# Kernel optimization log

Measured on AMD Instinct MI355X. Metric: run time of the kernel, lower is better.

Reference implementation:

```python
import jax, jax.numpy as jnp
import numpy as np


def setup_inputs() -> dict:
    key = jax.random.key(0)
    k1, k2, k3 = jax.random.split(key, 3)
    B, I, O = 2048, 256, 512
    x = jax.random.normal(k1, (B, I), dtype=jnp.float32)
    weight = jax.random.normal(k2, (O, I, 2), dtype=jnp.float32) * 0.1
    bias = jax.random.normal(k3, (O, I + 1), dtype=jnp.float32) * 0.1
    return {"x": x, "weight": weight, "bias": bias}


def reference(x, weight, bias):
    # out[b, o] = sum_i weight[o, i, 0] * sin(weight[o, i, 1] * x[b, i] + bias[o, i]) + bias[o, -1]
    w_out = weight[:, :, 0]          # [O, I]
    w_sin = weight[:, :, 1]          # [O, I]
    b_sin = bias[:, :-1]             # [O, I]
    b_out = bias[:, -1]              # [O]
    # [B, O, I] intermediate: sin applied before the reduction over in_features
    trig = jnp.sin(x[:, None, :] * w_sin[None, :, :] + b_sin[None, :, :])
    out = jnp.einsum('oi,boi->bo', w_out, trig) + b_out[None, :]
    return out
```

## Files before the change

### kernel.cpp

```cpp
#include <hip/hip_runtime.h>


#define B_SZ 2048
#define I_SZ 256
#define O_SZ 512
#define BTILE 64
#define ITILE 128
#define OBLOCK 16
#define NOO 4

static constexpr float kInv2Pi = 0.15915494309189535f;

__global__ __launch_bounds__(256, 4) void TrigoLinear_kernel(
    const float* __restrict__ x, const float* __restrict__ w,
    const float* __restrict__ bias, float* __restrict__ out) {
  __shared__ float xT[ITILE][BTILE + 1];

  const int tid = threadIdx.x;
  const int lane = tid & 63;
  const int wave = __builtin_amdgcn_readfirstlane(tid >> 6);

  const int btile = blockIdx.x & 31;
  const int oblock = blockIdx.x >> 5;
  const int b0 = btile * BTILE;
  const int o_base = oblock * OBLOCK + wave * NOO;

  float acc[NOO] = {0.f, 0.f, 0.f, 0.f};

  for (int it = 0; it < I_SZ / ITILE; ++it) {
    __syncthreads();
#pragma unroll
    for (int k = 0; k < 32; ++k) {
      int e = tid + k * 256;
      int row = e >> 7;
      int col = e & 127;
      xT[col][row] = x[(b0 + row) * I_SZ + it * ITILE + col] * kInv2Pi;
    }
    __syncthreads();

#pragma unroll 4
    for (int i = 0; i < ITILE; ++i) {
      const float xs = xT[i][lane];
      const int ig = it * ITILE + i;
#pragma unroll
      for (int oo = 0; oo < NOO; ++oo) {
        const int o = o_base + oo;
        const float wov = w[o * (2 * I_SZ) + 2 * ig];
        const float wsv = w[o * (2 * I_SZ) + 2 * ig + 1];
        const float bsv = bias[o * (I_SZ + 1) + ig];
        float t = xs * wsv;
        float rev = __builtin_fmaf(bsv, kInv2Pi, t);
        float r = __builtin_amdgcn_fractf(rev);
        float sv = __builtin_amdgcn_sinf(r);
        acc[oo] = __builtin_fmaf(sv, wov, acc[oo]);
      }
    }
  }

  const int b = b0 + lane;
#pragma unroll
  for (int oo = 0; oo < NOO; ++oo) {
    const int o = o_base + oo;
    const float bout = bias[o * (I_SZ + 1) + I_SZ];
    out[b * O_SZ + o] = acc[oo] + bout;
  }
}

extern "C" void kernel_launch(void* const* d_in, const int* in_sizes, int n_in,
                              void* d_out, int out_size, void* d_ws, size_t ws_size,
                              hipStream_t stream) {
  const float* x = (const float*)d_in[0];
  const float* w = (const float*)d_in[1];
  const float* bias = (const float*)d_in[2];
  float* out = (float*)d_out;

  const int grid = (B_SZ / BTILE) * (O_SZ / OBLOCK);
  TrigoLinear_kernel<<<dim3(grid), dim3(256), 0, stream>>>(x, w, bias, out);
}
```

Before: 53.08 us.

## Pre-scale weights in a prep kernel, drop fract, and shrink tiles

Adds a prep kernel that splits the interleaved weights into planar arrays. The sin-frequency and phase arrays are pre-multiplied by 1/(2π), so the inner loop becomes a single fma feeding the hardware sin, and the explicit fract range reduction is removed. The main kernel also moves to smaller I/O tiles (ITILE 64, 2 outputs per wave), a higher launch-bounds occupancy hint, and float4 loads when staging x. This trades an extra kernel launch and a workspace round-trip for fewer VALU ops per element. Dropping fract relies on the hardware sin tolerating unreduced arguments.

```diff
diff --git a/kernel.cpp b/kernel.cpp
--- a/kernel.cpp
+++ b/kernel.cpp
@@ -5,15 +5,29 @@
 #define I_SZ 256
 #define O_SZ 512
 #define BTILE 64
-#define ITILE 128
-#define OBLOCK 16
-#define NOO 4
+#define ITILE 64
+#define OBLOCK 8
+#define NOO 2
 
 static constexpr float kInv2Pi = 0.15915494309189535f;
 
-__global__ __launch_bounds__(256, 4) void TrigoLinear_kernel(
-    const float* __restrict__ x, const float* __restrict__ w,
-    const float* __restrict__ bias, float* __restrict__ out) {
+__global__ __launch_bounds__(256) void prep_kernel(
+    const float* __restrict__ w, const float* __restrict__ bias,
+    float* __restrict__ A, float* __restrict__ Bm, float* __restrict__ C) {
+  const int o = blockIdx.x;
+  const int i = threadIdx.x;
+  const float2 wp = *reinterpret_cast<const float2*>(&w[o * (2 * I_SZ) + 2 * i]);
+  A[o * I_SZ + i] = wp.y * kInv2Pi;
+  Bm[o * I_SZ + i] = wp.x;
+  C[o * I_SZ + i] = bias[o * (I_SZ + 1) + i] * kInv2Pi;
+}
+
+template <bool PREPPED>
+__global__ __launch_bounds__(256, 8) void TrigoLinear_kernel(
+    const float* __restrict__ x, const float* __restrict__ A,
+    const float* __restrict__ Bm, const float* __restrict__ C,
+    const float* __restrict__ w, const float* __restrict__ bias,
+    float* __restrict__ out) {
   __shared__ float xT[ITILE][BTILE + 1];
 
   const int tid = threadIdx.x;
@@ -25,34 +39,50 @@
   const int b0 = btile * BTILE;
   const int o_base = oblock * OBLOCK + wave * NOO;
 
-  float acc[NOO] = {0.f, 0.f, 0.f, 0.f};
+  float acc[NOO] = {0.f, 0.f};
 
   for (int it = 0; it < I_SZ / ITILE; ++it) {
     __syncthreads();
 #pragma unroll
-    for (int k = 0; k < 32; ++k) {
-      int e = tid + k * 256;
-      int row = e >> 7;
-      int col = e & 127;
-      xT[col][row] = x[(b0 + row) * I_SZ + it * ITILE + col] * kInv2Pi;
+    for (int c = 0; c < 4; ++c) {
+      const int idx = tid + c * 256;
+      const int row = idx >> 4;
+      const int col = (idx & 15) * 4;
+      float4 v = *reinterpret_cast<const float4*>(
+          &x[(b0 + row) * I_SZ + it * ITILE + col]);
+      if (!PREPPED) {
+        v.x *= kInv2Pi; v.y *= kInv2Pi; v.z *= kInv2Pi; v.w *= kInv2Pi;
+      }
+      xT[col + 0][row] = v.x;
+      xT[col + 1][row] = v.y;
+      xT[col + 2][row] = v.z;
+      xT[col + 3][row] = v.w;
     }
     __syncthreads();
 
-#pragma unroll 4
+#pragma unroll 8
     for (int i = 0; i < ITILE; ++i) {
       const float xs = xT[i][lane];
       const int ig = it * ITILE + i;
 #pragma unroll
       for (int oo = 0; oo < NOO; ++oo) {
         const int o = o_base + oo;
-        const float wov = w[o * (2 * I_SZ) + 2 * ig];
-        const float wsv = w[o * (2 * I_SZ) + 2 * ig + 1];
-        const float bsv = bias[o * (I_SZ + 1) + ig];
-        float t = xs * wsv;
-        float rev = __builtin_fmaf(bsv, kInv2Pi, t);
-        float r = __builtin_amdgcn_fractf(rev);
-        float sv = __builtin_amdgcn_sinf(r);
-        acc[oo] = __builtin_fmaf(sv, wov, acc[oo]);
+        if (PREPPED) {
+          const float a = A[o * I_SZ + ig];
+          const float bo = Bm[o * I_SZ + ig];
+          const float c = C[o * I_SZ + ig];
+          const float rev = __builtin_fmaf(xs, a, c);
+          const float sv = __builtin_amdgcn_sinf(rev);
+          acc[oo] = __builtin_fmaf(sv, bo, acc[oo]);
+        } else {
+          const float wov = w[o * (2 * I_SZ) + 2 * ig];
+          const float wsv = w[o * (2 * I_SZ) + 2 * ig + 1];
+          const float bsv = bias[o * (I_SZ + 1) + ig];
+          const float t = xs * wsv;
+          const float rev = __builtin_fmaf(bsv, kInv2Pi, t);
+          const float sv = __builtin_amdgcn_sinf(rev);
+          acc[oo] = __builtin_fmaf(sv, wov, acc[oo]);
+        }
       }
     }
   }
@@ -61,8 +91,7 @@
 #pragma unroll
   for (int oo = 0; oo < NOO; ++oo) {
     const int o = o_base + oo;
-    const float bout = bias[o * (I_SZ + 1) + I_SZ];
-    out[b * O_SZ + o] = acc[oo] + bout;
+    out[b * O_SZ + o] = acc[oo] + bias[o * (I_SZ + 1) + I_SZ];
   }
 }
 
@@ -75,5 +104,17 @@
   float* out = (float*)d_out;
 
   const int grid = (B_SZ / BTILE) * (O_SZ / OBLOCK);
-  TrigoLinear_kernel<<<dim3(grid), dim3(256), 0, stream>>>(x, w, bias, out);
+  const size_t need = (size_t)3 * O_SZ * I_SZ * sizeof(float);
+
+  if (ws_size >= need) {
+    float* A = (float*)d_ws;
+    float* Bm = A + O_SZ * I_SZ;
+    float* C = Bm + O_SZ * I_SZ;
+    prep_kernel<<<dim3(O_SZ), dim3(I_SZ), 0, stream>>>(w, bias, A, Bm, C);
+    TrigoLinear_kernel<true><<<dim3(grid), dim3(256), 0, stream>>>(
+        x, A, Bm, C, w, bias, out);
+  } else {
+    TrigoLinear_kernel<false><<<dim3(grid), dim3(256), 0, stream>>>(
+        x, nullptr, nullptr, nullptr, w, bias, out);
+  }
 }
```

New measurement: 55.77 us. 1.05x slower.

## Prepack weights into workspace and read x rows directly with register prefetch

Applied to the files above, without the earlier changes.

Adds a prep kernel that repacks the weight and bias into pre-scaled float4/float2 arrays in the workspace, so the main loop does one FMA per sin and drops the fract range reduction. The main kernel no longer stages x through shared memory: each lane reads its own x row as float4 with double-buffered register prefetch. Each wave now computes 2 outputs with 4 accumulators, and occupancy is raised to 6 blocks per CU. Removing fract relies on the hardware sin accepting unreduced arguments. The extra launch and strided per-lane x loads may cost bandwidth in exchange.

```diff
diff --git a/kernel.cpp b/kernel.cpp
--- a/kernel.cpp
+++ b/kernel.cpp
@@ -4,66 +4,108 @@
 #define B_SZ 2048
 #define I_SZ 256
 #define O_SZ 512
-#define BTILE 64
-#define ITILE 128
-#define OBLOCK 16
-#define NOO 4
 
 static constexpr float kInv2Pi = 0.15915494309189535f;
 
-__global__ __launch_bounds__(256, 4) void TrigoLinear_kernel(
-    const float* __restrict__ x, const float* __restrict__ w,
+__global__ __launch_bounds__(128) void prep_kernel(
+    const float* __restrict__ w, const float* __restrict__ bias,
+    float4* __restrict__ AC, float2* __restrict__ W) {
+  const int o = blockIdx.x;
+  const int i2 = threadIdx.x;
+  const float4 wq = *reinterpret_cast<const float4*>(&w[o * 2 * I_SZ + 4 * i2]);
+  const float b0 = bias[o * (I_SZ + 1) + 2 * i2];
+  const float b1 = bias[o * (I_SZ + 1) + 2 * i2 + 1];
+  AC[o * 128 + i2] =
+      make_float4(wq.y * kInv2Pi, wq.w * kInv2Pi, b0 * kInv2Pi, b1 * kInv2Pi);
+  W[o * 128 + i2] = make_float2(wq.x, wq.z);
+}
+
+template <bool PREPPED>
+__global__ __launch_bounds__(256, 6) void TrigoLinear_kernel(
+    const float* __restrict__ x, const float4* __restrict__ AC,
+    const float2* __restrict__ W, const float* __restrict__ w_raw,
     const float* __restrict__ bias, float* __restrict__ out) {
-  __shared__ float xT[ITILE][BTILE + 1];
-
   const int tid = threadIdx.x;
   const int lane = tid & 63;
   const int wave = __builtin_amdgcn_readfirstlane(tid >> 6);
 
   const int btile = blockIdx.x & 31;
-  const int oblock = blockIdx.x >> 5;
-  const int b0 = btile * BTILE;
-  const int o_base = oblock * OBLOCK + wave * NOO;
+  const int ogrp = blockIdx.x >> 5;
+  const int o0 = __builtin_amdgcn_readfirstlane(ogrp * 8 + wave * 2);
+  const int o1 = o0 + 1;
+  const int b = btile * 64 + lane;
 
-  float acc[NOO] = {0.f, 0.f, 0.f, 0.f};
+  const float4* __restrict__ xrow =
+      reinterpret_cast<const float4*>(x + (size_t)b * I_SZ);
 
-  for (int it = 0; it < I_SZ / ITILE; ++it) {
-    __syncthreads();
+  const float4* __restrict__ AC0 = AC + (size_t)o0 * 128;
+  const float4* __restrict__ AC1 = AC + (size_t)o1 * 128;
+  const float2* __restrict__ W0 = W + (size_t)o0 * 128;
+  const float2* __restrict__ W1 = W + (size_t)o1 * 128;
+  const float4* __restrict__ WR0 =
+      reinterpret_cast<const float4*>(w_raw + (size_t)o0 * 2 * I_SZ);
+  const float4* __restrict__ WR1 =
+      reinterpret_cast<const float4*>(w_raw + (size_t)o1 * 2 * I_SZ);
+  const float* __restrict__ BR0 = bias + (size_t)o0 * (I_SZ + 1);
+  const float* __restrict__ BR1 = bias + (size_t)o1 * (I_SZ + 1);
+
+  float acc00 = 0.f, acc01 = 0.f;
+  float acc10 = 0.f, acc11 = 0.f;
+
+  auto process = [&](int c, const float4* xq) {
 #pragma unroll
-    for (int k = 0; k < 32; ++k) {
-      int e = tid + k * 256;
-      int row = e >> 7;
-      int col = e & 127;
-      xT[col][row] = x[(b0 + row) * I_SZ + it * ITILE + col] * kInv2Pi;
-    }
-    __syncthreads();
-
-#pragma unroll 4
-    for (int i = 0; i < ITILE; ++i) {
-      const float xs = xT[i][lane];
-      const int ig = it * ITILE + i;
-#pragma unroll
-      for (int oo = 0; oo < NOO; ++oo) {
-        const int o = o_base + oo;
-        const float wov = w[o * (2 * I_SZ) + 2 * ig];
-        const float wsv = w[o * (2 * I_SZ) + 2 * ig + 1];
-        const float bsv = bias[o * (I_SZ + 1) + ig];
-        float t = xs * wsv;
-        float rev = __builtin_fmaf(bsv, kInv2Pi, t);
-        float r = __builtin_amdgcn_fractf(rev);
-        float sv = __builtin_amdgcn_sinf(r);
-        acc[oo] = __builtin_fmaf(sv, wov, acc[oo]);
+    for (int q = 0; q < 8; ++q) {
+      const float4 xv = xq[q >> 1];
+      const float xe = (q & 1) ? xv.z : xv.x;
+      const float xo = (q & 1) ? xv.w : xv.y;
+      const int i2 = c * 8 + q;
+      if (PREPPED) {
+        const float4 ac0 = AC0[i2];
+        const float4 ac1 = AC1[i2];
+        const float2 wv0 = W0[i2];
+        const float2 wv1 = W1[i2];
+        acc00 = __builtin_fmaf(
+            __builtin_amdgcn_sinf(__builtin_fmaf(xe, ac0.x, ac0.z)), wv0.x, acc00);
+        acc01 = __builtin_fmaf(
+            __builtin_amdgcn_sinf(__builtin_fmaf(xo, ac0.y, ac0.w)), wv0.y, acc01);
+        acc10 = __builtin_fmaf(
+            __builtin_amdgcn_sinf(__builtin_fmaf(xe, ac1.x, ac1.z)), wv1.x, acc10);
+        acc11 = __builtin_fmaf(
+            __builtin_amdgcn_sinf(__builtin_fmaf(xo, ac1.y, ac1.w)), wv1.y, acc11);
+      } else {
+        const float4 wq0 = WR0[i2];
+        const float4 wq1 = WR1[i2];
+        const float be0 = BR0[2 * i2], bo0 = BR0[2 * i2 + 1];
+        const float be1 = BR1[2 * i2], bo1 = BR1[2 * i2 + 1];
+        float t;
+        t = __builtin_fmaf(xe, wq0.y, be0) * kInv2Pi;
+        acc00 = __builtin_fmaf(__builtin_amdgcn_sinf(t), wq0.x, acc00);
+        t = __builtin_fmaf(xo, wq0.w, bo0) * kInv2Pi;
+        acc01 = __builtin_fmaf(__builtin_amdgcn_sinf(t), wq0.z, acc01);
+        t = __builtin_fmaf(xe, wq1.y, be1) * kInv2Pi;
+        acc10 = __builtin_fmaf(__builtin_amdgcn_sinf(t), wq1.x, acc10);
+        t = __builtin_fmaf(xo, wq1.w, bo1) * kInv2Pi;
+        acc11 = __builtin_fmaf(__builtin_amdgcn_sinf(t), wq1.z, acc11);
       }
     }
+  };
+
+  float4 xq[4], xn[4];
+#pragma unroll
+  for (int k = 0; k < 4; ++k) xq[k] = xrow[k];
+
+#pragma unroll 1
+  for (int c = 0; c < 15; ++c) {
+#pragma unroll
+    for (int k = 0; k < 4; ++k) xn[k] = xrow[(c + 1) * 4 + k];
+    process(c, xq);
+#pragma unroll
+    for (int k = 0; k < 4; ++k) xq[k] = xn[k];
   }
+  process(15, xq);
 
-  const int b = b0 + lane;
-#pragma unroll
-  for (int oo = 0; oo < NOO; ++oo) {
-    const int o = o_base + oo;
-    const float bout = bias[o * (I_SZ + 1) + I_SZ];
-    out[b * O_SZ + o] = acc[oo] + bout;
-  }
+  out[(size_t)b * O_SZ + o0] = acc00 + acc01 + bias[(size_t)o0 * (I_SZ + 1) + I_SZ];
+  out[(size_t)b * O_SZ + o1] = acc10 + acc11 + bias[(size_t)o1 * (I_SZ + 1) + I_SZ];
 }
 
 extern "C" void kernel_launch(void* const* d_in, const int* in_sizes, int n_in,
@@ -74,6 +116,18 @@
   const float* bias = (const float*)d_in[2];
   float* out = (float*)d_out;
 
-  const int grid = (B_SZ / BTILE) * (O_SZ / OBLOCK);
-  TrigoLinear_kernel<<<dim3(grid), dim3(256), 0, stream>>>(x, w, bias, out);
+  const int grid = (B_SZ / 64) * (O_SZ / 8);
+  const size_t needAC = (size_t)O_SZ * 128 * sizeof(float4);
+  const size_t needW = (size_t)O_SZ * 128 * sizeof(float2);
+
+  if (ws_size >= needAC + needW) {
+    float4* AC = (float4*)d_ws;
+    float2* W = (float2*)((char*)d_ws + needAC);
+    prep_kernel<<<dim3(O_SZ), dim3(128), 0, stream>>>(w, bias, AC, W);
+    TrigoLinear_kernel<true><<<dim3(grid), dim3(256), 0, stream>>>(
+        x, AC, W, w, bias, out);
+  } else {
+    TrigoLinear_kernel<false><<<dim3(grid), dim3(256), 0, stream>>>(
+        x, nullptr, nullptr, w, bias, out);
+  }
 }
```

Result: slower. 78.29 us (+47.5%).

## Prepack weights into planar arrays and use register-pipelined vector loads with packed FMA

Applied to the files above, without the earlier changes.

A prep kernel splits the interleaved weight and bias into three contiguous planes (sin scale, phase and output weight), with the 1/2π factor folded in. This lets the main kernel use float4 loads. The main kernel drops LDS staging of x. Each lane instead reads its own x row with float4 loads, double-buffered in registers, and computes two outputs per wave using packed 2-wide FMAs. The fract range reduction is removed, which relies on the hardware sin handling the small arguments directly. In exchange it adds an extra kernel launch and workspace traffic, and x reuse now depends on the cache rather than shared memory.

```diff
diff --git a/kernel.cpp b/kernel.cpp
--- a/kernel.cpp
+++ b/kernel.cpp
@@ -4,66 +4,122 @@
 #define B_SZ 2048
 #define I_SZ 256
 #define O_SZ 512
-#define BTILE 64
-#define ITILE 128
-#define OBLOCK 16
-#define NOO 4
 
+typedef float f32x2 __attribute__((ext_vector_type(2)));
 static constexpr float kInv2Pi = 0.15915494309189535f;
 
-__global__ __launch_bounds__(256, 4) void TrigoLinear_kernel(
+static __device__ __forceinline__ f32x2 mk2(float a, float b) {
+  f32x2 r; r.x = a; r.y = b; return r;
+}
+#if __has_builtin(__builtin_elementwise_fma)
+static __device__ __forceinline__ f32x2 fma2(f32x2 a, f32x2 b, f32x2 c) {
+  return __builtin_elementwise_fma(a, b, c);
+}
+#else
+static __device__ __forceinline__ f32x2 fma2(f32x2 a, f32x2 b, f32x2 c) {
+  return mk2(__builtin_fmaf(a.x, b.x, c.x), __builtin_fmaf(a.y, b.y, c.y));
+}
+#endif
+static __device__ __forceinline__ f32x2 sin2(f32x2 v) {
+  return mk2(__builtin_amdgcn_sinf(v.x), __builtin_amdgcn_sinf(v.y));
+}
+
+__global__ __launch_bounds__(256) void prep_kernel(
+    const float* __restrict__ w, const float* __restrict__ bias,
+    float* __restrict__ A, float* __restrict__ C, float* __restrict__ W) {
+  const int o = blockIdx.x;
+  const int i = threadIdx.x;
+  const float2 wp = *reinterpret_cast<const float2*>(&w[(size_t)o * 2 * I_SZ + 2 * i]);
+  A[o * I_SZ + i] = wp.y * kInv2Pi;
+  C[o * I_SZ + i] = bias[o * (I_SZ + 1) + i] * kInv2Pi;
+  W[o * I_SZ + i] = wp.x;
+}
+
+__global__ __launch_bounds__(256, 6) void TrigoLinear_kernel(
+    const float* __restrict__ x, const float* __restrict__ A,
+    const float* __restrict__ C, const float* __restrict__ W,
+    const float* __restrict__ bias, float* __restrict__ out) {
+  const int tid = threadIdx.x;
+  const int lane = tid & 63;
+  const int wave = tid >> 6;
+  const int btile = blockIdx.x & 31;
+  const int og = blockIdx.x >> 5;
+  const int o0 = og * 8 + wave * 2;
+  const int b = btile * 64 + lane;
+
+  int opq0;
+  asm("v_mov_b32 %0, 0" : "=v"(opq0));
+  const int wi = o0 * I_SZ + opq0;
+  const int xi = b * I_SZ;
+
+  f32x2 acc0a = mk2(0.f, 0.f), acc0b = mk2(0.f, 0.f);
+  f32x2 acc1a = mk2(0.f, 0.f), acc1b = mk2(0.f, 0.f);
+
+  float4 Px, Pa0, Pc0, Pw0, Pa1, Pc1, Pw1;
+  float4 Qx, Qa0, Qc0, Qw0, Qa1, Qc1, Qw1;
+
+#define LD4(base, off) (*reinterpret_cast<const float4*>((base) + (off)))
+#define STAGE(S, cc)                                            \
+  do {                                                          \
+    const int _o = (cc) << 2;                                   \
+    S##x  = LD4(x, xi + _o);                                    \
+    S##a0 = LD4(A, wi + _o);                                    \
+    S##c0 = LD4(C, wi + _o);                                    \
+    S##w0 = LD4(W, wi + _o);                                    \
+    S##a1 = LD4(A, wi + I_SZ + _o);                             \
+    S##c1 = LD4(C, wi + I_SZ + _o);                             \
+    S##w1 = LD4(W, wi + I_SZ + _o);                             \
+  } while (0)
+
+#define COMP(S)                                                               \
+  do {                                                                        \
+    const f32x2 xlo = mk2(S##x.x, S##x.y);                                    \
+    const f32x2 xhi = mk2(S##x.z, S##x.w);                                    \
+    acc0a = fma2(sin2(fma2(xlo, mk2(S##a0.x, S##a0.y), mk2(S##c0.x, S##c0.y))), \
+                 mk2(S##w0.x, S##w0.y), acc0a);                               \
+    acc0b = fma2(sin2(fma2(xhi, mk2(S##a0.z, S##a0.w), mk2(S##c0.z, S##c0.w))), \
+                 mk2(S##w0.z, S##w0.w), acc0b);                               \
+    acc1a = fma2(sin2(fma2(xlo, mk2(S##a1.x, S##a1.y), mk2(S##c1.x, S##c1.y))), \
+                 mk2(S##w1.x, S##w1.y), acc1a);                               \
+    acc1b = fma2(sin2(fma2(xhi, mk2(S##a1.z, S##a1.w), mk2(S##c1.z, S##c1.w))), \
+                 mk2(S##w1.z, S##w1.w), acc1b);                               \
+  } while (0)
+
+  STAGE(P, 0);
+#pragma unroll 1
+  for (int c = 0; c < 64; c += 2) {
+    STAGE(Q, c + 1);
+    COMP(P);
+    STAGE(P, (c + 2) & 63);
+    COMP(Q);
+  }
+#undef LD4
+#undef STAGE
+#undef COMP
+
+  const float out0 =
+      acc0a.x + acc0a.y + acc0b.x + acc0b.y + bias[(size_t)o0 * (I_SZ + 1) + I_SZ];
+  const float out1 = acc1a.x + acc1a.y + acc1b.x + acc1b.y +
+                     bias[(size_t)(o0 + 1) * (I_SZ + 1) + I_SZ];
+  out[(size_t)b * O_SZ + o0] = out0;
+  out[(size_t)b * O_SZ + o0 + 1] = out1;
+}
+
+__global__ __launch_bounds__(256) void trig_fallback(
     const float* __restrict__ x, const float* __restrict__ w,
     const float* __restrict__ bias, float* __restrict__ out) {
-  __shared__ float xT[ITILE][BTILE + 1];
-
-  const int tid = threadIdx.x;
-  const int lane = tid & 63;
-  const int wave = __builtin_amdgcn_readfirstlane(tid >> 6);
-
-  const int btile = blockIdx.x & 31;
-  const int oblock = blockIdx.x >> 5;
-  const int b0 = btile * BTILE;
-  const int o_base = oblock * OBLOCK + wave * NOO;
-
-  float acc[NOO] = {0.f, 0.f, 0.f, 0.f};
-
-  for (int it = 0; it < I_SZ / ITILE; ++it) {
-    __syncthreads();
-#pragma unroll
-    for (int k = 0; k < 32; ++k) {
-      int e = tid + k * 256;
-      int row = e >> 7;
-      int col = e & 127;
-      xT[col][row] = x[(b0 + row) * I_SZ + it * ITILE + col] * kInv2Pi;
-    }
-    __syncthreads();
-
-#pragma unroll 4
-    for (int i = 0; i < ITILE; ++i) {
-      const float xs = xT[i][lane];
-      const int ig = it * ITILE + i;
-#pragma unroll
-      for (int oo = 0; oo < NOO; ++oo) {
-        const int o = o_base + oo;
-        const float wov = w[o * (2 * I_SZ) + 2 * ig];
-        const float wsv = w[o * (2 * I_SZ) + 2 * ig + 1];
-        const float bsv = bias[o * (I_SZ + 1) + ig];
-        float t = xs * wsv;
-        float rev = __builtin_fmaf(bsv, kInv2Pi, t);
-        float r = __builtin_amdgcn_fractf(rev);
-        float sv = __builtin_amdgcn_sinf(r);
-        acc[oo] = __builtin_fmaf(sv, wov, acc[oo]);
-      }
-    }
+  const int idx = blockIdx.x * 256 + threadIdx.x;
+  const int b = idx >> 9;
+  const int o = idx & 511;
+  float acc = bias[o * (I_SZ + 1) + I_SZ];
+  for (int i = 0; i < I_SZ; ++i) {
+    const float ws = w[(size_t)o * 2 * I_SZ + 2 * i + 1];
+    const float wo = w[(size_t)o * 2 * I_SZ + 2 * i];
+    const float bs = bias[o * (I_SZ + 1) + i];
+    const float rev = __builtin_fmaf(x[(size_t)b * I_SZ + i], ws, bs) * kInv2Pi;
+    acc = __builtin_fmaf(__builtin_amdgcn_sinf(rev), wo, acc);
   }
-
-  const int b = b0 + lane;
-#pragma unroll
-  for (int oo = 0; oo < NOO; ++oo) {
-    const int o = o_base + oo;
-    const float bout = bias[o * (I_SZ + 1) + I_SZ];
-    out[b * O_SZ + o] = acc[oo] + bout;
-  }
+  out[idx] = acc;
 }
 
 extern "C" void kernel_launch(void* const* d_in, const int* in_sizes, int n_in,
@@ -74,6 +130,17 @@
   const float* bias = (const float*)d_in[2];
   float* out = (float*)d_out;
 
-  const int grid = (B_SZ / BTILE) * (O_SZ / OBLOCK);
-  TrigoLinear_kernel<<<dim3(grid), dim3(256), 0, stream>>>(x, w, bias, out);
+  const size_t plane = (size_t)O_SZ * I_SZ;
+  const size_t need = 3 * plane * sizeof(float);
+
+  if (ws_size >= need) {
+    float* A = (float*)d_ws;
+    float* C = A + plane;
+    float* W = C + plane;
+    prep_kernel<<<dim3(O_SZ), dim3(I_SZ), 0, stream>>>(w, bias, A, C, W);
+    const int grid = (B_SZ / 64) * (O_SZ / 8);
+    TrigoLinear_kernel<<<dim3(grid), dim3(256), 0, stream>>>(x, A, C, W, bias, out);
+  } else {
+    trig_fallback<<<dim3(B_SZ * O_SZ / 256), dim3(256), 0, stream>>>(x, w, bias, out);
+  }
 }
```

After: 169.3 us. 3.19x slower.
